# Optimization experiments

Hardware: AMD Instinct MI355X
Metric: run time of the kernel (lower is better)

## Reference

```python
import jax, jax.numpy as jnp
import numpy as np

B, N, K, C = 16, 1024, 64, 128
TEMPERATURE = 0.07


def _l2_normalize(x, eps=1e-12):
    # matches torch F.normalize(dim=-1): x / max(||x||, eps)
    n = jnp.linalg.norm(x, axis=-1, keepdims=True)
    return x / jnp.maximum(n, eps)


def setup_inputs() -> dict:
    key = jax.random.key(0)
    k1, k2, k3, k4 = jax.random.split(key, 4)
    q = jax.random.normal(k1, (B, N, C), dtype=jnp.float32)
    k = jax.random.normal(k2, (B, N, C), dtype=jnp.float32)
    positive_indices = jax.random.randint(k3, (B, N), 0, N)
    negative_indices = jax.random.randint(k4, (B, N, K), 0, N)
    return {"q": q, "k": k,
            "positive_indices": positive_indices,
            "negative_indices": negative_indices}


def reference(q, k, positive_indices, negative_indices):
    qn = _l2_normalize(q)                                   # (B,N,C)
    kn = _l2_normalize(k)                                   # (B,N,C)

    pos_valid = positive_indices >= 0                       # (B,N)
    pos_idx = jnp.where(pos_valid, positive_indices, 0)
    positive = jnp.take_along_axis(kn, pos_idx[..., None], axis=1)  # (B,N,C)
    pos_sim = jnp.sum(qn * positive, axis=-1) / TEMPERATURE          # (B,N)

    neg_valid = negative_indices >= 0                       # (B,N,K)
    neg_idx = jnp.where(neg_valid, negative_indices, 0)
    # batched ragged gather of negatives: (B,N,K,C)
    negs = jax.vmap(lambda kb, idx: kb[idx])(kn, neg_idx)
    neg_sim = jnp.einsum('bnc,bnkc->bnk', qn, negs) / TEMPERATURE    # (B,N,K)
    neg_sim = jnp.where(neg_valid, neg_sim, -jnp.inf)

    # cross-entropy with label 0 over [pos, negs]:
    # loss = logsumexp(logits) - pos_sim
    logits = jnp.concatenate([pos_sim[..., None], neg_sim], axis=-1)  # (B,N,1+K)
    per_patch = jax.nn.logsumexp(logits, axis=-1) - pos_sim           # (B,N)

    total = jnp.sum(jnp.where(pos_valid, per_patch, 0.0))
    count = jnp.sum(pos_valid)
    return jnp.where(count > 0, total / jnp.maximum(count, 1), 0.0)
```

## Files before the change

### kernel.cpp

```cpp
#include <hip/hip_runtime.h>
#include <math.h>

#define B_ 16
#define N_ 1024
#define K_ 64
#define C_ 128
#define INV_T 14.285714285714286f
#define NBLK_MAIN 2048

__device__ __forceinline__ float waveReduceSum(float v) {
#pragma unroll
    for (int off = 32; off > 0; off >>= 1)
        v += __shfl_xor(v, off, 64);
    return v;
}

__device__ __forceinline__ float waveReduceMax(float v) {
#pragma unroll
    for (int off = 32; off > 0; off >>= 1)
        v = fmaxf(v, __shfl_xor(v, off, 64));
    return v;
}

__global__ __launch_bounds__(256) void knorm_kernel(const float* __restrict__ k,
                                                    float* __restrict__ inv_k) {
    const int lane = threadIdx.x & 63;
    const int wid  = threadIdx.x >> 6;
    const int base = blockIdx.x * 16 + wid * 4;
#pragma unroll
    for (int r = 0; r < 4; ++r) {
        const int row = base + r;
        const float2 kv = *(const float2*)(k + (size_t)row * C_ + 2 * lane);
        float ss = waveReduceSum(kv.x * kv.x + kv.y * kv.y);
        if (lane == 0) inv_k[row] = 1.0f / fmaxf(sqrtf(ss), 1e-12f);
    }
}

__global__ __launch_bounds__(256, 4) void infonce_kernel(
    const float* __restrict__ q, const float* __restrict__ k,
    const int* __restrict__ pos_idx, const int* __restrict__ neg_idx,
    const float* __restrict__ inv_k, float* __restrict__ partials) {
    __shared__ float q_lds[4][C_];
    __shared__ float wave_tot[4], wave_cnt[4];

    const int lane = threadIdx.x & 63;
    const int wid  = threadIdx.x >> 6;
    const int g    = lane >> 3;
    const int s    = lane & 7;

    const int batch = blockIdx.x & 15;
    const int chunk = blockIdx.x >> 4;
    const int rbase = chunk * 8 + wid * 2;

    const float* kb    = k + (size_t)batch * (N_ * C_);
    const float* invkb = inv_k + batch * N_;

    float tot = 0.0f, cnt = 0.0f;

#pragma unroll
    for (int r = 0; r < 2; ++r) {
        const int n   = rbase + r;
        const int row = batch * N_ + n;
        const float* qrow = q + (size_t)row * C_;

        const float2 qv = *(const float2*)(qrow + 2 * lane);
        *(float2*)(&q_lds[wid][2 * lane]) = qv;

        const int  pidx = pos_idx[row];
        const bool pval = pidx >= 0;
        const int  p0   = pval ? pidx : 0;

        const int my_nidx = neg_idx[(size_t)row * K_ + lane];

        int nidx[8];
#pragma unroll
        for (int p = 0; p < 8; ++p) nidx[p] = __shfl(my_nidx, p * 8 + g, 64);

        float4 q4[4];
#pragma unroll
        for (int i = 0; i < 4; ++i)
            q4[i] = *(const float4*)(&q_lds[wid][i * 32 + s * 4]);

        float d[9];
#pragma unroll
        for (int p = 0; p < 9; ++p) {
            const float* kr;
            if (p < 8) kr = kb + (size_t)(nidx[p] >= 0 ? nidx[p] : 0) * C_;
            else       kr = (g == 0) ? (kb + (size_t)p0 * C_) : qrow;
            float dot = 0.0f;
#pragma unroll
            for (int i = 0; i < 4; ++i) {
                const float4 kv = *(const float4*)(kr + i * 32 + s * 4);
                dot = fmaf(kv.x, q4[i].x, dot);
                dot = fmaf(kv.y, q4[i].y, dot);
                dot = fmaf(kv.z, q4[i].z, dot);
                dot = fmaf(kv.w, q4[i].w, dot);
            }
            dot += __shfl_xor(dot, 1, 64);
            dot += __shfl_xor(dot, 2, 64);
            dot += __shfl_xor(dot, 4, 64);
            d[p] = dot;
        }

        const float pos_dot = __int_as_float(__builtin_amdgcn_readlane(__float_as_int(d[8]), 0));
        const float qss     = __int_as_float(__builtin_amdgcn_readlane(__float_as_int(d[8]), 8));
        const float scale   = (1.0f / fmaxf(sqrtf(qss), 1e-12f)) * INV_T;
        const float pos_sim = pos_dot * scale * invkb[p0];

        float simv[8];
#pragma unroll
        for (int p = 0; p < 8; ++p) {
            const bool nv = nidx[p] >= 0;
            const float ik = invkb[nv ? nidx[p] : 0];
            simv[p] = nv ? d[p] * scale * ik : -INFINITY;
        }

        float m = pos_sim;
#pragma unroll
        for (int p = 0; p < 8; ++p) m = fmaxf(m, simv[p]);
        m = waveReduceMax(m);
        float ssum = 0.0f;
        if (s == 0) {
#pragma unroll
            for (int p = 0; p < 8; ++p) ssum += __expf(simv[p] - m);
        }
        ssum = waveReduceSum(ssum) + __expf(pos_sim - m);
        const float per_patch = m + __logf(ssum) - pos_sim;

        if (pval) { tot += per_patch; cnt += 1.0f; }
    }

    if (lane == 0) { wave_tot[wid] = tot; wave_cnt[wid] = cnt; }
    __syncthreads();
    if (threadIdx.x == 0) {
        partials[2 * blockIdx.x]     = wave_tot[0] + wave_tot[1] + wave_tot[2] + wave_tot[3];
        partials[2 * blockIdx.x + 1] = wave_cnt[0] + wave_cnt[1] + wave_cnt[2] + wave_cnt[3];
    }
}

__global__ __launch_bounds__(256) void finalize_kernel(const float* __restrict__ partials,
                                                       float* __restrict__ out, int nblocks) {
    __shared__ float st[256], sc[256];
    float t = 0.0f, c = 0.0f;
    for (int i = threadIdx.x; i < nblocks; i += 256) {
        t += partials[2 * i];
        c += partials[2 * i + 1];
    }
    st[threadIdx.x] = t;
    sc[threadIdx.x] = c;
    __syncthreads();
    for (int off = 128; off > 0; off >>= 1) {
        if (threadIdx.x < off) {
            st[threadIdx.x] += st[threadIdx.x + off];
            sc[threadIdx.x] += sc[threadIdx.x + off];
        }
        __syncthreads();
    }
    if (threadIdx.x == 0) {
        const float cntv = sc[0];
        out[0] = (cntv > 0.0f) ? st[0] / fmaxf(cntv, 1.0f) : 0.0f;
    }
}

extern "C" void kernel_launch(void* const* d_in, const int* in_sizes, int n_in,
                              void* d_out, int out_size, void* d_ws, size_t ws_size,
                              hipStream_t stream) {
    const float* q   = (const float*)d_in[0];
    const float* k   = (const float*)d_in[1];
    const int*   pos = (const int*)d_in[2];
    const int*   neg = (const int*)d_in[3];
    float* out = (float*)d_out;
    float* ws  = (float*)d_ws;

    float* partials = ws;
    float* inv_k    = ws + 2 * NBLK_MAIN;

    knorm_kernel<<<1024, 256, 0, stream>>>(k, inv_k);
    infonce_kernel<<<NBLK_MAIN, 256, 0, stream>>>(q, k, pos, neg, inv_k, partials);
    finalize_kernel<<<1, 256, 0, stream>>>(partials, out, NBLK_MAIN);
}
```

Measured before the change: 102.1 us.

## Pre-normalize q and k into bf16 buffers and gather bf16 rows

A prepass now normalizes both q and k and stores them as bf16, so the main kernel gathers half-width rows and no longer needs per-row inverse norms, the q self-dot, or the LDS staging of q. This halves the bytes moved by the random gathers of negatives, which dominate the main kernel. In exchange the prepass reads all of q and writes two bf16 copies, and the loss is computed at bf16 input precision, which may shift the result slightly relative to the fp32 reference.

```diff
diff --git a/kernel.cpp b/kernel.cpp
--- a/kernel.cpp
+++ b/kernel.cpp
@@ -22,25 +22,38 @@
     return v;
 }
 
-__global__ __launch_bounds__(256) void knorm_kernel(const float* __restrict__ k,
-                                                    float* __restrict__ inv_k) {
+__device__ __forceinline__ unsigned short f2bf(float x) {
+    unsigned u = __float_as_uint(x);
+    return (unsigned short)((u + 0x7fffu + ((u >> 16) & 1u)) >> 16);
+}
+__device__ __forceinline__ float bflo(unsigned u) { return __uint_as_float(u << 16); }
+__device__ __forceinline__ float bfhi(unsigned u) { return __uint_as_float(u & 0xffff0000u); }
+
+__global__ __launch_bounds__(256) void normalize_kernel(
+    const float* __restrict__ q, const float* __restrict__ k,
+    unsigned short* __restrict__ qn, unsigned short* __restrict__ kn) {
     const int lane = threadIdx.x & 63;
     const int wid  = threadIdx.x >> 6;
     const int base = blockIdx.x * 16 + wid * 4;
 #pragma unroll
     for (int r = 0; r < 4; ++r) {
         const int row = base + r;
-        const float2 kv = *(const float2*)(k + (size_t)row * C_ + 2 * lane);
-        float ss = waveReduceSum(kv.x * kv.x + kv.y * kv.y);
-        if (lane == 0) inv_k[row] = 1.0f / fmaxf(sqrtf(ss), 1e-12f);
+        const bool is_q = row < (B_ * N_);
+        const int  rr   = is_q ? row : row - B_ * N_;
+        const float* src = (is_q ? q : k) + (size_t)rr * C_;
+        unsigned short* dst = (is_q ? qn : kn) + (size_t)rr * C_;
+        const float2 v = *(const float2*)(src + 2 * lane);
+        const float ss = waveReduceSum(v.x * v.x + v.y * v.y);
+        const float inv = 1.0f / fmaxf(sqrtf(ss), 1e-12f);
+        ushort2 o; o.x = f2bf(v.x * inv); o.y = f2bf(v.y * inv);
+        *(ushort2*)(dst + 2 * lane) = o;
     }
 }
 
 __global__ __launch_bounds__(256, 4) void infonce_kernel(
-    const float* __restrict__ q, const float* __restrict__ k,
+    const unsigned short* __restrict__ qn, const unsigned short* __restrict__ kn,
     const int* __restrict__ pos_idx, const int* __restrict__ neg_idx,
-    const float* __restrict__ inv_k, float* __restrict__ partials) {
-    __shared__ float q_lds[4][C_];
+    float* __restrict__ partials) {
     __shared__ float wave_tot[4], wave_cnt[4];
 
     const int lane = threadIdx.x & 63;
@@ -52,8 +65,7 @@
     const int chunk = blockIdx.x >> 4;
     const int rbase = chunk * 8 + wid * 2;
 
-    const float* kb    = k + (size_t)batch * (N_ * C_);
-    const float* invkb = inv_k + batch * N_;
+    const unsigned short* kb = kn + (size_t)batch * (N_ * C_);
 
     float tot = 0.0f, cnt = 0.0f;
 
@@ -61,40 +73,45 @@
     for (int r = 0; r < 2; ++r) {
         const int n   = rbase + r;
         const int row = batch * N_ + n;
-        const float* qrow = q + (size_t)row * C_;
 
-        const float2 qv = *(const float2*)(qrow + 2 * lane);
-        *(float2*)(&q_lds[wid][2 * lane]) = qv;
+        const unsigned short* qrow = qn + (size_t)row * C_;
+        float qf[16];
+#pragma unroll
+        for (int i = 0; i < 2; ++i) {
+            const uint4 qu = *(const uint4*)(qrow + i * 64 + s * 8);
+            qf[i*8+0] = bflo(qu.x); qf[i*8+1] = bfhi(qu.x);
+            qf[i*8+2] = bflo(qu.y); qf[i*8+3] = bfhi(qu.y);
+            qf[i*8+4] = bflo(qu.z); qf[i*8+5] = bfhi(qu.z);
+            qf[i*8+6] = bflo(qu.w); qf[i*8+7] = bfhi(qu.w);
+        }
 
         const int  pidx = pos_idx[row];
         const bool pval = pidx >= 0;
         const int  p0   = pval ? pidx : 0;
 
         const int my_nidx = neg_idx[(size_t)row * K_ + lane];
-
         int nidx[8];
 #pragma unroll
         for (int p = 0; p < 8; ++p) nidx[p] = __shfl(my_nidx, p * 8 + g, 64);
 
-        float4 q4[4];
-#pragma unroll
-        for (int i = 0; i < 4; ++i)
-            q4[i] = *(const float4*)(&q_lds[wid][i * 32 + s * 4]);
-
         float d[9];
 #pragma unroll
         for (int p = 0; p < 9; ++p) {
-            const float* kr;
-            if (p < 8) kr = kb + (size_t)(nidx[p] >= 0 ? nidx[p] : 0) * C_;
-            else       kr = (g == 0) ? (kb + (size_t)p0 * C_) : qrow;
+            const unsigned short* kr =
+                (p < 8) ? kb + (size_t)(nidx[p] >= 0 ? nidx[p] : 0) * C_
+                        : kb + (size_t)p0 * C_;
             float dot = 0.0f;
 #pragma unroll
-            for (int i = 0; i < 4; ++i) {
-                const float4 kv = *(const float4*)(kr + i * 32 + s * 4);
-                dot = fmaf(kv.x, q4[i].x, dot);
-                dot = fmaf(kv.y, q4[i].y, dot);
-                dot = fmaf(kv.z, q4[i].z, dot);
-                dot = fmaf(kv.w, q4[i].w, dot);
+            for (int i = 0; i < 2; ++i) {
+                const uint4 ku = *(const uint4*)(kr + i * 64 + s * 8);
+                dot = fmaf(bflo(ku.x), qf[i*8+0], dot);
+                dot = fmaf(bfhi(ku.x), qf[i*8+1], dot);
+                dot = fmaf(bflo(ku.y), qf[i*8+2], dot);
+                dot = fmaf(bfhi(ku.y), qf[i*8+3], dot);
+                dot = fmaf(bflo(ku.z), qf[i*8+4], dot);
+                dot = fmaf(bfhi(ku.z), qf[i*8+5], dot);
+                dot = fmaf(bflo(ku.w), qf[i*8+6], dot);
+                dot = fmaf(bfhi(ku.w), qf[i*8+7], dot);
             }
             dot += __shfl_xor(dot, 1, 64);
             dot += __shfl_xor(dot, 2, 64);
@@ -102,18 +119,12 @@
             d[p] = dot;
         }
 
-        const float pos_dot = __int_as_float(__builtin_amdgcn_readlane(__float_as_int(d[8]), 0));
-        const float qss     = __int_as_float(__builtin_amdgcn_readlane(__float_as_int(d[8]), 8));
-        const float scale   = (1.0f / fmaxf(sqrtf(qss), 1e-12f)) * INV_T;
-        const float pos_sim = pos_dot * scale * invkb[p0];
+        const float pos_sim = d[8] * INV_T;
 
         float simv[8];
 #pragma unroll
-        for (int p = 0; p < 8; ++p) {
-            const bool nv = nidx[p] >= 0;
-            const float ik = invkb[nv ? nidx[p] : 0];
-            simv[p] = nv ? d[p] * scale * ik : -INFINITY;
-        }
+        for (int p = 0; p < 8; ++p)
+            simv[p] = (nidx[p] >= 0) ? d[p] * INV_T : -INFINITY;
 
         float m = pos_sim;
 #pragma unroll
@@ -170,12 +181,13 @@
     const int*   pos = (const int*)d_in[2];
     const int*   neg = (const int*)d_in[3];
     float* out = (float*)d_out;
-    float* ws  = (float*)d_ws;
 
-    float* partials = ws;
-    float* inv_k    = ws + 2 * NBLK_MAIN;
+    float* wsf = (float*)d_ws;
+    float* partials = wsf;
+    unsigned short* qn = (unsigned short*)(wsf + 8192);
+    unsigned short* kn = qn + (size_t)B_ * N_ * C_;
 
-    knorm_kernel<<<1024, 256, 0, stream>>>(k, inv_k);
-    infonce_kernel<<<NBLK_MAIN, 256, 0, stream>>>(q, k, pos, neg, inv_k, partials);
+    normalize_kernel<<<2048, 256, 0, stream>>>(q, k, qn, kn);
+    infonce_kernel<<<NBLK_MAIN, 256, 0, stream>>>(qn, kn, pos, neg, partials);
     finalize_kernel<<<1, 256, 0, stream>>>(partials, out, NBLK_MAIN);
 }
```

After: 90.12 us. 1.13x faster.
